# Kernel tuning notes

Hardware: AMD Instinct MI355X
Metric: run time of the kernel (lower is better)

## Reference

```python
import jax, jax.numpy as jnp
import numpy as np

K_HOPS = 3  # spektral TAGConv default
BN_EPS = 1e-3  # keras BatchNormalization default epsilon


def _propagate(x, edge_src, edge_dst, edge_weight, n_nodes):
    # y[dst] += w * x[src]  (sparse adjacency @ x)
    msg = x[edge_src] * edge_weight[:, None]
    return jax.ops.segment_sum(msg, edge_dst, num_segments=n_nodes)


def _tag_conv(x, edge_src, edge_dst, edge_weight, W, b):
    n = x.shape[0]
    hops = [x]
    h = x
    for _ in range(K_HOPS):
        h = _propagate(h, edge_src, edge_dst, edge_weight, n)
        hops.append(h)
    # concat hops along features then dense combine: [N, F*(K+1)] @ [F*(K+1), C]
    return jnp.concatenate(hops, axis=-1) @ W + b


def setup_inputs() -> dict:
    key = jax.random.key(0)
    ks = jax.random.split(key, 6)
    N, F, E, H, L = 20000, 2000, 640000, 128, 15
    x = jax.random.normal(ks[0], (N, F), dtype=jnp.float32)
    edge_src = jax.random.randint(ks[1], (E,), 0, N, dtype=jnp.int32)
    edge_dst = jax.random.randint(ks[2], (E,), 0, N, dtype=jnp.int32)
    # normalized adjacency weights, roughly 1/avg_degree scale
    edge_weight = jax.random.uniform(ks[3], (E,), dtype=jnp.float32) / 32.0
    W1 = jax.random.normal(ks[4], (F * (K_HOPS + 1), H), dtype=jnp.float32) * (1.0 / np.sqrt(F * (K_HOPS + 1)))
    b1 = jnp.zeros((H,), dtype=jnp.float32)
    gamma = jnp.ones((H,), dtype=jnp.float32)
    beta = jnp.zeros((H,), dtype=jnp.float32)
    moving_mean = jnp.zeros((H,), dtype=jnp.float32)
    moving_var = jnp.ones((H,), dtype=jnp.float32)
    W2 = jax.random.normal(ks[5], (H * (K_HOPS + 1), L), dtype=jnp.float32) * (1.0 / np.sqrt(H * (K_HOPS + 1)))
    b2 = jnp.zeros((L,), dtype=jnp.float32)
    return {"x": x, "edge_src": edge_src, "edge_dst": edge_dst, "edge_weight": edge_weight,
            "W1": W1, "b1": b1, "gamma": gamma, "beta": beta,
            "moving_mean": moving_mean, "moving_var": moving_var, "W2": W2, "b2": b2}


def reference(x, edge_src, edge_dst, edge_weight, W1, b1, gamma, beta,
              moving_mean, moving_var, W2, b2):
    # training=False: Dropout is identity, BN uses moving statistics
    h = _tag_conv(x, edge_src, edge_dst, edge_weight, W1, b1)
    h = (h - moving_mean) * jax.lax.rsqrt(moving_var + BN_EPS) * gamma + beta
    h = jax.nn.relu(h)
    z = _tag_conv(h, edge_src, edge_dst, edge_weight, W2, b2)
    return z
```

## Files before the change

kernel.cpp:

```cpp
#include <hip/hip_runtime.h>
#include <hip/hip_bf16.h>
#include <cstdint>
#include <cstddef>

#define N_NODES 20000
#define F_IN    2000
#define H_DIM   128
#define L_DIM   15
#define K_PAD   2048
#define N1      512
#define BM      128
#define BN      128
#define BK      32
#define I_TILES 157

typedef __attribute__((ext_vector_type(4))) float f32x4;
typedef __attribute__((ext_vector_type(8))) short s16x8;
typedef __attribute__((ext_vector_type(8))) unsigned short u16x8;

__device__ __forceinline__ unsigned short f2bf(float f) {
  unsigned int u = __float_as_uint(f);
  u += 0x7fff + ((u >> 16) & 1);
  return (unsigned short)(u >> 16);
}

__device__ __forceinline__ unsigned int pkbf(float a, float b) {
  union { __hip_bfloat162 h; unsigned int u; } cv;
  cv.h = __float22bfloat162_rn(make_float2(a, b));
  return cv.u;
}

__device__ __forceinline__ float2 bf2f(unsigned int u) {
  float2 r;
  r.x = __uint_as_float(u << 16);
  r.y = __uint_as_float(u & 0xffff0000u);
  return r;
}

__global__ __launch_bounds__(256) void k_cvt_x(const float* __restrict__ x,
                                               unsigned short* __restrict__ xb) {
  unsigned int t = blockIdx.x * 256u + threadIdx.x;
  unsigned int row = t >> 8;
  unsigned int colB = (t & 255u) * 8u;
  u16x8 o = {0, 0, 0, 0, 0, 0, 0, 0};
  if (colB < F_IN) {
    const float4 a = *(const float4*)(x + (size_t)row * F_IN + colB);
    const float4 b = *(const float4*)(x + (size_t)row * F_IN + colB + 4);
    o[0] = f2bf(a.x); o[1] = f2bf(a.y); o[2] = f2bf(a.z); o[3] = f2bf(a.w);
    o[4] = f2bf(b.x); o[5] = f2bf(b.y); o[6] = f2bf(b.z); o[7] = f2bf(b.w);
  }
  *(u16x8*)(xb + (size_t)t * 8) = o;
}

__global__ __launch_bounds__(256) void k_cvt_w1(const float* __restrict__ W1,
                                                unsigned short* __restrict__ bt) {
  __shared__ unsigned short tile[128 * 67];
  const int hop = blockIdx.x >> 5;
  const int k0  = (blockIdx.x & 31) * 64;
  const int t = threadIdx.x;
#pragma unroll
  for (int it = 0; it < 8; ++it) {
    int f4 = it * 256 + t;
    int r  = f4 >> 5;
    int c4 = f4 & 31;
    int k = k0 + r;
    float4 v = make_float4(0.f, 0.f, 0.f, 0.f);
    if (k < F_IN) v = *(const float4*)(W1 + (size_t)(hop * F_IN + k) * H_DIM + c4 * 4);
    tile[(c4 * 4 + 0) * 67 + r] = f2bf(v.x);
    tile[(c4 * 4 + 1) * 67 + r] = f2bf(v.y);
    tile[(c4 * 4 + 2) * 67 + r] = f2bf(v.z);
    tile[(c4 * 4 + 3) * 67 + r] = f2bf(v.w);
  }
  __syncthreads();
  const int c = t >> 1, kh = (t & 1) * 32;
  unsigned short* dst = bt + (size_t)(hop * 128 + c) * K_PAD + k0 + kh;
  const unsigned short* srcp = tile + c * 67 + kh;
#pragma unroll
  for (int q = 0; q < 4; ++q) {
    u16x8 o;
#pragma unroll
    for (int e = 0; e < 8; ++e) o[e] = srcp[q * 8 + e];
    *(u16x8*)(dst + q * 8) = o;
  }
}

__global__ __launch_bounds__(256) void k_gemm1(const unsigned short* __restrict__ A,
                                               const unsigned short* __restrict__ B,
                                               float* __restrict__ C0) {
  __shared__ unsigned short As[BM * BK];
  __shared__ unsigned short Bs[BN * BK];
  const int b = blockIdx.x;
  const int i_tile = (b & 7) + 8 * (b >> 6);
  const int mid = (b >> 3) & 7;
  const int j_tile = mid & 3;
  const int ks = mid >> 2;
  if (i_tile >= I_TILES) return;
  const int rowA0 = i_tile * BM;
  const int colB0 = j_tile * BN;
  const int tid  = threadIdx.x;
  const int lane = tid & 63;
  const int wave = tid >> 6;
  const int wm = (wave >> 1) * 64;
  const int wn = (wave & 1) * 64;
  const int quad = lane >> 4;
  const int l15  = lane & 15;
  f32x4 acc[4][4] = {};

  const int kend = ks ? F_IN : 1024;
  for (int kt = ks * 1024; kt < kend; kt += BK) {
#pragma unroll
    for (int r = 0; r < 2; ++r) {
      int c = r * 256 + tid;
      int row = c >> 2;
      int kc = (c & 3) * 8;
      const unsigned short* ga = A + (size_t)(rowA0 + row) * K_PAD + kt + kc;
      __builtin_amdgcn_global_load_lds((const __attribute__((address_space(1))) void*)ga,
                                       (__attribute__((address_space(3))) void*)(As + c * 8),
                                       16, 0, 0);
      const unsigned short* gb = B + (size_t)(colB0 + row) * K_PAD + kt + kc;
      __builtin_amdgcn_global_load_lds((const __attribute__((address_space(1))) void*)gb,
                                       (__attribute__((address_space(3))) void*)(Bs + c * 8),
                                       16, 0, 0);
    }
    __syncthreads();
    s16x8 af[4], bfr[4];
#pragma unroll
    for (int i = 0; i < 4; ++i)
      af[i] = *(const s16x8*)(As + (wm + i * 16 + l15) * BK + quad * 8);
#pragma unroll
    for (int j = 0; j < 4; ++j)
      bfr[j] = *(const s16x8*)(Bs + (wn + j * 16 + l15) * BK + quad * 8);
#pragma unroll
    for (int i = 0; i < 4; ++i)
#pragma unroll
      for (int j = 0; j < 4; ++j)
        acc[i][j] = __builtin_amdgcn_mfma_f32_16x16x32_bf16(af[i], bfr[j], acc[i][j], 0, 0, 0);
    __syncthreads();
  }

#pragma unroll
  for (int i = 0; i < 4; ++i) {
    int row0 = rowA0 + wm + i * 16 + quad * 4;
#pragma unroll
    for (int j = 0; j < 4; ++j) {
      int col = colB0 + wn + j * 16 + l15;
#pragma unroll
      for (int r = 0; r < 4; ++r) {
        int row = row0 + r;
        if (row < N_NODES)
          unsafeAtomicAdd(&C0[(size_t)row * N1 + col], acc[i][j][r]);
      }
    }
  }
}

__global__ __launch_bounds__(256) void k_mkYb3(const float* __restrict__ C0,
                                               unsigned short* __restrict__ Yb3) {
  unsigned int t = blockIdx.x * 256u + threadIdx.x;
  unsigned int row = t >> 5;
  unsigned int c4 = (t & 31u) * 4u;
  float4 s = *(const float4*)(C0 + (size_t)row * N1 + 384 + c4);
  *(uint2*)(Yb3 + (size_t)row * H_DIM + c4) = make_uint2(pkbf(s.x, s.y), pkbf(s.z, s.w));
}

__global__ __launch_bounds__(256) void k_hist(const int* __restrict__ dst,
                                              int* __restrict__ deg, int E) {
  int i = blockIdx.x * 256 + threadIdx.x;
  int e = i * 4;
  if (e + 4 <= E) {
    int4 d4 = *(const int4*)(dst + e);
    atomicAdd(&deg[d4.x], 1); atomicAdd(&deg[d4.y], 1);
    atomicAdd(&deg[d4.z], 1); atomicAdd(&deg[d4.w], 1);
  } else {
    for (; e < E; ++e) atomicAdd(&deg[dst[e]], 1);
  }
}

__global__ __launch_bounds__(1024) void k_scan(const int* __restrict__ deg,
                                               int* __restrict__ rowStart,
                                               int* __restrict__ cursor) {
  __shared__ int sums[1024];
  const int t = threadIdx.x;
  const int chunk = (N_NODES + 1023) / 1024;
  int lo = t * chunk;
  int hi = lo + chunk; if (hi > N_NODES) hi = N_NODES;
  int s = 0;
  for (int i = lo; i < hi; ++i) s += deg[i];
  sums[t] = s;
  __syncthreads();
  for (int off = 1; off < 1024; off <<= 1) {
    int v = sums[t];
    int u = (t >= off) ? sums[t - off] : 0;
    __syncthreads();
    sums[t] = v + u;
    __syncthreads();
  }
  int run = sums[t] - s;
  for (int i = lo; i < hi; ++i) {
    rowStart[i] = run; cursor[i] = run; run += deg[i];
  }
  if (t == 1023) rowStart[N_NODES] = run;
}

__global__ __launch_bounds__(256) void k_scatter(const int* __restrict__ src,
                                                 const int* __restrict__ dst,
                                                 const float* __restrict__ w,
                                                 int* cursor,
                                                 int2* __restrict__ eSW, int E) {
  int e = blockIdx.x * 256 + threadIdx.x;
  if (e >= E) return;
  int p = atomicAdd(&cursor[dst[e]], 1);
  eSW[p] = make_int2(src[e], __float_as_int(w[e]));
}

__global__ __launch_bounds__(256) void k_prop128c(const int* __restrict__ rowStart,
    const int2* __restrict__ eSW,
    const unsigned short* __restrict__ gsrc,
    const float* __restrict__ addv, int addStride, int addOff,
    unsigned short* __restrict__ outb, float* __restrict__ outf,
    const float* __restrict__ b1, const float* __restrict__ gamma,
    const float* __restrict__ beta, const float* __restrict__ mean,
    const float* __restrict__ var, int doBN) {
  __shared__ float red[2][128];
  const int lane = threadIdx.x & 63;
  const int wave = threadIdx.x >> 6;
  const int rb = wave >> 1;
  const int h  = wave & 1;
  const int d = blockIdx.x * 2 + rb;
  const int s0 = rowStart[d], s1 = rowStart[d + 1];
  const int c2 = lane * 2;
  float ax = 0.f, ay = 0.f;
  int j = s0 + h;
  for (; j + 6 < s1; j += 8) {
    int2 e0 = eSW[j], e1 = eSW[j + 2], e2 = eSW[j + 4], e3 = eSW[j + 6];
    unsigned int g0 = *(const unsigned int*)(gsrc + (size_t)e0.x * H_DIM + c2);
    unsigned int g1 = *(const unsigned int*)(gsrc + (size_t)e1.x * H_DIM + c2);
    unsigned int g2 = *(const unsigned int*)(gsrc + (size_t)e2.x * H_DIM + c2);
    unsigned int g3 = *(const unsigned int*)(gsrc + (size_t)e3.x * H_DIM + c2);
    float2 v0 = bf2f(g0), v1 = bf2f(g1), v2 = bf2f(g2), v3 = bf2f(g3);
    float w0 = __int_as_float(e0.y), w1 = __int_as_float(e1.y);
    float w2 = __int_as_float(e2.y), w3 = __int_as_float(e3.y);
    ax = fmaf(w0, v0.x, ax); ay = fmaf(w0, v0.y, ay);
    ax = fmaf(w1, v1.x, ax); ay = fmaf(w1, v1.y, ay);
    ax = fmaf(w2, v2.x, ax); ay = fmaf(w2, v2.y, ay);
    ax = fmaf(w3, v3.x, ax); ay = fmaf(w3, v3.y, ay);
  }
  for (; j < s1; j += 2) {
    int2 e = eSW[j];
    float2 v = bf2f(*(const unsigned int*)(gsrc + (size_t)e.x * H_DIM + c2));
    float w = __int_as_float(e.y);
    ax = fmaf(w, v.x, ax); ay = fmaf(w, v.y, ay);
  }
  if (h) { red[rb][c2] = ax; red[rb][c2 + 1] = ay; }
  __syncthreads();
  if (h) return;
  ax += red[rb][c2]; ay += red[rb][c2 + 1];
  float2 av = *(const float2*)(addv + (size_t)d * addStride + addOff + c2);
  float r0 = av.x + ax, r1 = av.y + ay;
  if (doBN) {
    float2 bb = *(const float2*)(b1 + c2);
    float2 gg = *(const float2*)(gamma + c2);
    float2 be = *(const float2*)(beta + c2);
    float2 mm = *(const float2*)(mean + c2);
    float2 vv = *(const float2*)(var + c2);
    r0 = (r0 + bb.x - mm.x) * rsqrtf(vv.x + 1e-3f) * gg.x + be.x;
    r1 = (r1 + bb.y - mm.y) * rsqrtf(vv.y + 1e-3f) * gg.y + be.y;
    r0 = r0 > 0.f ? r0 : 0.f;
    r1 = r1 > 0.f ? r1 : 0.f;
    *(float2*)(outf + (size_t)d * H_DIM + c2) = make_float2(r0, r1);
  } else {
    *(unsigned int*)(outb + (size_t)d * H_DIM + c2) = pkbf(r0, r1);
  }
}

__global__ __launch_bounds__(256) void k_gemm2(const float* __restrict__ Hh,
                                               const float* __restrict__ W2,
                                               float* __restrict__ Y2) {
  __shared__ float w2s[512 * 15];
  for (int i = threadIdx.x; i < 512 * 15; i += 256) w2s[i] = W2[i];
  __syncthreads();
  const int c = threadIdx.x & 63;
  const int d = blockIdx.x * 4 + (threadIdx.x >> 6);
  if (c >= 60 || d >= N_NODES) return;
  const int hop = c / 15, j = c % 15;
  const float4* hr4 = (const float4*)(Hh + (size_t)d * H_DIM);
  float acc = 0.f;
#pragma unroll 8
  for (int k4 = 0; k4 < 32; ++k4) {
    float4 h = hr4[k4];
    const float* wp = w2s + ((hop << 7) + k4 * 4) * 15 + j;
    acc = fmaf(h.x, wp[0],  acc);
    acc = fmaf(h.y, wp[15], acc);
    acc = fmaf(h.z, wp[30], acc);
    acc = fmaf(h.w, wp[45], acc);
  }
  Y2[(size_t)d * 60 + c] = acc;
}

__global__ __launch_bounds__(256) void k_prop15(const int* __restrict__ rowStart,
    const int2* __restrict__ eSW,
    const float* __restrict__ in, int inStride, int inOff,
    const float* __restrict__ addv, int addStride, int addOff,
    const float* __restrict__ bias, float* __restrict__ out) {
  const int f = threadIdx.x & 15;
  const int d = blockIdx.x * 16 + (threadIdx.x >> 4);
  if (f >= 15) return;
  const int s0 = rowStart[d], s1 = rowStart[d + 1];
  float acc = 0.f;
  int j = s0;
  for (; j + 4 <= s1; j += 4) {
    int2 e0 = eSW[j], e1 = eSW[j + 1], e2 = eSW[j + 2], e3 = eSW[j + 3];
    float v0 = in[(size_t)e0.x * inStride + inOff + f];
    float v1 = in[(size_t)e1.x * inStride + inOff + f];
    float v2 = in[(size_t)e2.x * inStride + inOff + f];
    float v3 = in[(size_t)e3.x * inStride + inOff + f];
    acc = fmaf(__int_as_float(e0.y), v0, acc);
    acc = fmaf(__int_as_float(e1.y), v1, acc);
    acc = fmaf(__int_as_float(e2.y), v2, acc);
    acc = fmaf(__int_as_float(e3.y), v3, acc);
  }
  for (; j < s1; ++j) {
    int2 e = eSW[j];
    acc = fmaf(__int_as_float(e.y), in[(size_t)e.x * inStride + inOff + f], acc);
  }
  float b = bias ? bias[f] : 0.f;
  out[(size_t)d * 15 + f] = addv[(size_t)d * addStride + addOff + f] + acc + b;
}

extern "C" void kernel_launch(void* const* d_in, const int* in_sizes, int n_in,
                              void* d_out, int out_size, void* d_ws, size_t ws_size,
                              hipStream_t stream) {
  const float* x     = (const float*)d_in[0];
  const int*   esrc  = (const int*)d_in[1];
  const int*   edst  = (const int*)d_in[2];
  const float* ew    = (const float*)d_in[3];
  const float* W1    = (const float*)d_in[4];
  const float* b1    = (const float*)d_in[5];
  const float* gamma = (const float*)d_in[6];
  const float* beta  = (const float*)d_in[7];
  const float* mmean = (const float*)d_in[8];
  const float* mvar  = (const float*)d_in[9];
  const float* W2    = (const float*)d_in[10];
  const float* b2    = (const float*)d_in[11];
  const int E = in_sizes[1];
  char* ws = (char*)d_ws;

  unsigned short* xb  = (unsigned short*)(ws);
  float*          C0  = (float*)(ws + 81920000);
  unsigned short* w1r = (unsigned short*)(ws + 122880000);
  int2*           eSW = (int2*)(ws + 124977152);
  int*       deg      = (int*)(ws + 130097152);
  int*       rowStart = (int*)(ws + 130177280);
  int*       cursor   = (int*)(ws + 130257408);
  unsigned short* Yb3 = (unsigned short*)(ws);
  unsigned short* P   = (unsigned short*)(ws + 5120000);
  unsigned short* Q   = (unsigned short*)(ws + 10240000);
  float*          Hb  = (float*)(ws + 15360000);
  float*          Y2  = (float*)(ws + 25600000);
  float*          zP  = (float*)(ws + 30400000);
  float*          zQ  = (float*)(ws + 31600000);
  float*          Y   = C0;
  float*          zout = (float*)d_out;

  hipMemsetAsync(deg, 0, N_NODES * sizeof(int), stream);
  hipMemsetAsync(C0, 0, (size_t)N_NODES * N1 * sizeof(float), stream);

  k_hist<<<(E / 4 + 255) / 256 + 1, 256, 0, stream>>>(edst, deg, E);
  k_scan<<<1, 1024, 0, stream>>>(deg, rowStart, cursor);
  k_scatter<<<(E + 255) / 256, 256, 0, stream>>>(esrc, edst, ew, cursor, eSW, E);

  k_cvt_x<<<(N_NODES * K_PAD / 8) / 256, 256, 0, stream>>>(x, xb);
  k_cvt_w1<<<128, 256, 0, stream>>>(W1, w1r);
  k_gemm1<<<1280, 256, 0, stream>>>(xb, w1r, C0);
  k_mkYb3<<<(N_NODES * 32) / 256, 256, 0, stream>>>(C0, Yb3);

  k_prop128c<<<N_NODES / 2, 256, 0, stream>>>(rowStart, eSW, Yb3, Y, N1, 2 * H_DIM,
                                              P, nullptr, b1, gamma, beta, mmean, mvar, 0);
  k_prop128c<<<N_NODES / 2, 256, 0, stream>>>(rowStart, eSW, P, Y, N1, 1 * H_DIM,
                                              Q, nullptr, b1, gamma, beta, mmean, mvar, 0);
  k_prop128c<<<N_NODES / 2, 256, 0, stream>>>(rowStart, eSW, Q, Y, N1, 0,
                                              nullptr, Hb, b1, gamma, beta, mmean, mvar, 1);

  k_gemm2<<<N_NODES / 4, 256, 0, stream>>>(Hb, W2, Y2);
  k_prop15<<<N_NODES / 16, 256, 0, stream>>>(rowStart, eSW, Y2, 60, 45, Y2, 60, 30, nullptr, zP);
  k_prop15<<<N_NODES / 16, 256, 0, stream>>>(rowStart, eSW, zP, 15, 0, Y2, 60, 15, nullptr, zQ);
  k_prop15<<<N_NODES / 16, 256, 0, stream>>>(rowStart, eSW, zQ, 15, 0, Y2, 60, 0, b2, zout);
}
```

Before: 643.3 us.

## Drop split-K atomics in gemm1, fuse bf16 output, restructure propagation kernel

The first GEMM no longer splits K across two blocks with atomic adds into a zeroed buffer. Each block now covers the full K range and writes plain stores, with the fourth column tile written directly as bf16, so the memset and the separate conversion kernel go away. The 128-wide propagation kernel now gives one wave per node, with lanes split into two halves reducing by shuffle instead of shared memory, and it software-pipelines the edge and gather loads with 4-wide loads per lane. The cost is half as many GEMM blocks, which means less parallelism and longer per-block K loops, plus higher register pressure in the pipelined gather.

```diff
diff --git a/kernel.cpp b/kernel.cpp
--- a/kernel.cpp
+++ b/kernel.cpp
@@ -8,7 +8,7 @@
 #define H_DIM   128
 #define L_DIM   15
 #define K_PAD   2048
-#define N1      512
+#define YS      384
 #define BM      128
 #define BN      128
 #define BK      32
@@ -86,14 +86,13 @@
 
 __global__ __launch_bounds__(256) void k_gemm1(const unsigned short* __restrict__ A,
                                                const unsigned short* __restrict__ B,
-                                               float* __restrict__ C0) {
+                                               float* __restrict__ Y,
+                                               unsigned short* __restrict__ Yb3) {
   __shared__ unsigned short As[BM * BK];
   __shared__ unsigned short Bs[BN * BK];
   const int b = blockIdx.x;
-  const int i_tile = (b & 7) + 8 * (b >> 6);
-  const int mid = (b >> 3) & 7;
-  const int j_tile = mid & 3;
-  const int ks = mid >> 2;
+  const int i_tile = (b & 7) + 8 * (b >> 5);
+  const int j_tile = (b >> 3) & 3;
   if (i_tile >= I_TILES) return;
   const int rowA0 = i_tile * BM;
   const int colB0 = j_tile * BN;
@@ -106,8 +105,7 @@
   const int l15  = lane & 15;
   f32x4 acc[4][4] = {};
 
-  const int kend = ks ? F_IN : 1024;
-  for (int kt = ks * 1024; kt < kend; kt += BK) {
+  for (int kt = 0; kt < K_PAD; kt += BK) {
 #pragma unroll
     for (int r = 0; r < 2; ++r) {
       int c = r * 256 + tid;
@@ -143,24 +141,19 @@
     int row0 = rowA0 + wm + i * 16 + quad * 4;
 #pragma unroll
     for (int j = 0; j < 4; ++j) {
-      int col = colB0 + wn + j * 16 + l15;
+      int col16 = wn + j * 16 + l15;
 #pragma unroll
       for (int r = 0; r < 4; ++r) {
         int row = row0 + r;
-        if (row < N_NODES)
-          unsafeAtomicAdd(&C0[(size_t)row * N1 + col], acc[i][j][r]);
+        if (row < N_NODES) {
+          if (j_tile < 3)
+            Y[(size_t)row * YS + colB0 + col16] = acc[i][j][r];
+          else
+            Yb3[(size_t)row * H_DIM + col16] = f2bf(acc[i][j][r]);
+        }
       }
     }
   }
-}
-
-__global__ __launch_bounds__(256) void k_mkYb3(const float* __restrict__ C0,
-                                               unsigned short* __restrict__ Yb3) {
-  unsigned int t = blockIdx.x * 256u + threadIdx.x;
-  unsigned int row = t >> 5;
-  unsigned int c4 = (t & 31u) * 4u;
-  float4 s = *(const float4*)(C0 + (size_t)row * N1 + 384 + c4);
-  *(uint2*)(Yb3 + (size_t)row * H_DIM + c4) = make_uint2(pkbf(s.x, s.y), pkbf(s.z, s.w));
 }
 
 __global__ __launch_bounds__(256) void k_hist(const int* __restrict__ dst,
@@ -213,7 +206,7 @@
   eSW[p] = make_int2(src[e], __float_as_int(w[e]));
 }
 
-__global__ __launch_bounds__(256) void k_prop128c(const int* __restrict__ rowStart,
+__global__ __launch_bounds__(256) void k_prop128d(const int* __restrict__ rowStart,
     const int2* __restrict__ eSW,
     const unsigned short* __restrict__ gsrc,
     const float* __restrict__ addv, int addStride, int addOff,
@@ -221,55 +214,87 @@
     const float* __restrict__ b1, const float* __restrict__ gamma,
     const float* __restrict__ beta, const float* __restrict__ mean,
     const float* __restrict__ var, int doBN) {
-  __shared__ float red[2][128];
   const int lane = threadIdx.x & 63;
   const int wave = threadIdx.x >> 6;
-  const int rb = wave >> 1;
-  const int h  = wave & 1;
-  const int d = blockIdx.x * 2 + rb;
+  const int h   = lane >> 5;
+  const int sub = lane & 31;
+  const int d = blockIdx.x * 4 + wave;
   const int s0 = rowStart[d], s1 = rowStart[d + 1];
-  const int c2 = lane * 2;
-  float ax = 0.f, ay = 0.f;
-  int j = s0 + h;
-  for (; j + 6 < s1; j += 8) {
-    int2 e0 = eSW[j], e1 = eSW[j + 2], e2 = eSW[j + 4], e3 = eSW[j + 6];
-    unsigned int g0 = *(const unsigned int*)(gsrc + (size_t)e0.x * H_DIM + c2);
-    unsigned int g1 = *(const unsigned int*)(gsrc + (size_t)e1.x * H_DIM + c2);
-    unsigned int g2 = *(const unsigned int*)(gsrc + (size_t)e2.x * H_DIM + c2);
-    unsigned int g3 = *(const unsigned int*)(gsrc + (size_t)e3.x * H_DIM + c2);
-    float2 v0 = bf2f(g0), v1 = bf2f(g1), v2 = bf2f(g2), v3 = bf2f(g3);
-    float w0 = __int_as_float(e0.y), w1 = __int_as_float(e1.y);
-    float w2 = __int_as_float(e2.y), w3 = __int_as_float(e3.y);
-    ax = fmaf(w0, v0.x, ax); ay = fmaf(w0, v0.y, ay);
-    ax = fmaf(w1, v1.x, ax); ay = fmaf(w1, v1.y, ay);
-    ax = fmaf(w2, v2.x, ax); ay = fmaf(w2, v2.y, ay);
-    ax = fmaf(w3, v3.x, ax); ay = fmaf(w3, v3.y, ay);
-  }
-  for (; j < s1; j += 2) {
-    int2 e = eSW[j];
-    float2 v = bf2f(*(const unsigned int*)(gsrc + (size_t)e.x * H_DIM + c2));
+  f32x4 acc = {0.f, 0.f, 0.f, 0.f};
+
+  const int nb = (s1 - s0) >> 3;
+  int j = s0;
+  int2 ed0[4], ed1[4];
+  uint2 g0[4];
+  if (nb > 0) {
+#pragma unroll
+    for (int i = 0; i < 4; ++i) ed0[i] = eSW[j + 2 * i + h];
+#pragma unroll
+    for (int i = 0; i < 4; ++i)
+      g0[i] = *(const uint2*)(gsrc + (size_t)ed0[i].x * H_DIM + sub * 4);
+#pragma unroll
+    for (int i = 0; i < 4; ++i)
+      ed1[i] = (nb > 1) ? eSW[j + 8 + 2 * i + h] : ed0[i];
+  }
+  for (int bb = 0; bb < nb; ++bb) {
+    uint2 g1[4];
+    if (bb + 1 < nb) {
+#pragma unroll
+      for (int i = 0; i < 4; ++i)
+        g1[i] = *(const uint2*)(gsrc + (size_t)ed1[i].x * H_DIM + sub * 4);
+    }
+    int2 ed2[4];
+    if (bb + 2 < nb) {
+#pragma unroll
+      for (int i = 0; i < 4; ++i) ed2[i] = eSW[j + 16 + 2 * i + h];
+    }
+#pragma unroll
+    for (int i = 0; i < 4; ++i) {
+      float w = __int_as_float(ed0[i].y);
+      float2 lo = bf2f(g0[i].x), hi = bf2f(g0[i].y);
+      acc.x = fmaf(w, lo.x, acc.x); acc.y = fmaf(w, lo.y, acc.y);
+      acc.z = fmaf(w, hi.x, acc.z); acc.w = fmaf(w, hi.y, acc.w);
+    }
+#pragma unroll
+    for (int i = 0; i < 4; ++i) { ed0[i] = ed1[i]; g0[i] = g1[i]; }
+    if (bb + 2 < nb) {
+#pragma unroll
+      for (int i = 0; i < 4; ++i) ed1[i] = ed2[i];
+    }
+    j += 8;
+  }
+  for (int t = s0 + nb * 8 + h; t < s1; t += 2) {
+    int2 e = eSW[t];
+    uint2 g = *(const uint2*)(gsrc + (size_t)e.x * H_DIM + sub * 4);
     float w = __int_as_float(e.y);
-    ax = fmaf(w, v.x, ax); ay = fmaf(w, v.y, ay);
-  }
-  if (h) { red[rb][c2] = ax; red[rb][c2 + 1] = ay; }
-  __syncthreads();
+    float2 lo = bf2f(g.x), hi = bf2f(g.y);
+    acc.x = fmaf(w, lo.x, acc.x); acc.y = fmaf(w, lo.y, acc.y);
+    acc.z = fmaf(w, hi.x, acc.z); acc.w = fmaf(w, hi.y, acc.w);
+  }
+  acc.x += __shfl_xor(acc.x, 32);
+  acc.y += __shfl_xor(acc.y, 32);
+  acc.z += __shfl_xor(acc.z, 32);
+  acc.w += __shfl_xor(acc.w, 32);
   if (h) return;
-  ax += red[rb][c2]; ay += red[rb][c2 + 1];
-  float2 av = *(const float2*)(addv + (size_t)d * addStride + addOff + c2);
-  float r0 = av.x + ax, r1 = av.y + ay;
+  const int c4 = sub * 4;
+  float4 av = *(const float4*)(addv + (size_t)d * addStride + addOff + c4);
+  float r0 = av.x + acc.x, r1 = av.y + acc.y;
+  float r2 = av.z + acc.z, r3 = av.w + acc.w;
   if (doBN) {
-    float2 bb = *(const float2*)(b1 + c2);
-    float2 gg = *(const float2*)(gamma + c2);
-    float2 be = *(const float2*)(beta + c2);
-    float2 mm = *(const float2*)(mean + c2);
-    float2 vv = *(const float2*)(var + c2);
+    float4 bb = *(const float4*)(b1 + c4);
+    float4 gg = *(const float4*)(gamma + c4);
+    float4 be = *(const float4*)(beta + c4);
+    float4 mm = *(const float4*)(mean + c4);
+    float4 vv = *(const float4*)(var + c4);
     r0 = (r0 + bb.x - mm.x) * rsqrtf(vv.x + 1e-3f) * gg.x + be.x;
     r1 = (r1 + bb.y - mm.y) * rsqrtf(vv.y + 1e-3f) * gg.y + be.y;
-    r0 = r0 > 0.f ? r0 : 0.f;
-    r1 = r1 > 0.f ? r1 : 0.f;
-    *(float2*)(outf + (size_t)d * H_DIM + c2) = make_float2(r0, r1);
+    r2 = (r2 + bb.z - mm.z) * rsqrtf(vv.z + 1e-3f) * gg.z + be.z;
+    r3 = (r3 + bb.w - mm.w) * rsqrtf(vv.w + 1e-3f) * gg.w + be.w;
+    r0 = r0 > 0.f ? r0 : 0.f; r1 = r1 > 0.f ? r1 : 0.f;
+    r2 = r2 > 0.f ? r2 : 0.f; r3 = r3 > 0.f ? r3 : 0.f;
+    *(float4*)(outf + (size_t)d * H_DIM + c4) = make_float4(r0, r1, r2, r3);
   } else {
-    *(unsigned int*)(outb + (size_t)d * H_DIM + c2) = pkbf(r0, r1);
+    *(uint2*)(outb + (size_t)d * H_DIM + c4) = make_uint2(pkbf(r0, r1), pkbf(r2, r3));
   }
 }
 
@@ -346,24 +371,22 @@
   char* ws = (char*)d_ws;
 
   unsigned short* xb  = (unsigned short*)(ws);
-  float*          C0  = (float*)(ws + 81920000);
-  unsigned short* w1r = (unsigned short*)(ws + 122880000);
-  int2*           eSW = (int2*)(ws + 124977152);
-  int*       deg      = (int*)(ws + 130097152);
-  int*       rowStart = (int*)(ws + 130177280);
-  int*       cursor   = (int*)(ws + 130257408);
-  unsigned short* Yb3 = (unsigned short*)(ws);
-  unsigned short* P   = (unsigned short*)(ws + 5120000);
-  unsigned short* Q   = (unsigned short*)(ws + 10240000);
-  float*          Hb  = (float*)(ws + 15360000);
-  float*          Y2  = (float*)(ws + 25600000);
-  float*          zP  = (float*)(ws + 30400000);
-  float*          zQ  = (float*)(ws + 31600000);
-  float*          Y   = C0;
+  float*          Y   = (float*)(ws + 81920000);
+  unsigned short* Yb3 = (unsigned short*)(ws + 112640000);
+  unsigned short* w1r = (unsigned short*)(ws + 117760000);
+  int2*           eSW = (int2*)(ws + 119857152);
+  int*       deg      = (int*)(ws + 124977152);
+  int*       rowStart = (int*)(ws + 125057280);
+  int*       cursor   = (int*)(ws + 125137408);
+  unsigned short* P   = (unsigned short*)(ws);
+  unsigned short* Q   = (unsigned short*)(ws + 5120000);
+  float*          Hb  = (float*)(ws + 10240000);
+  float*          Y2  = (float*)(ws + 20480000);
+  float*          zP  = (float*)(ws + 25280000);
+  float*          zQ  = (float*)(ws + 26480000);
   float*          zout = (float*)d_out;
 
   hipMemsetAsync(deg, 0, N_NODES * sizeof(int), stream);
-  hipMemsetAsync(C0, 0, (size_t)N_NODES * N1 * sizeof(float), stream);
 
   k_hist<<<(E / 4 + 255) / 256 + 1, 256, 0, stream>>>(edst, deg, E);
   k_scan<<<1, 1024, 0, stream>>>(deg, rowStart, cursor);
@@ -371,14 +394,13 @@
 
   k_cvt_x<<<(N_NODES * K_PAD / 8) / 256, 256, 0, stream>>>(x, xb);
   k_cvt_w1<<<128, 256, 0, stream>>>(W1, w1r);
-  k_gemm1<<<1280, 256, 0, stream>>>(xb, w1r, C0);
-  k_mkYb3<<<(N_NODES * 32) / 256, 256, 0, stream>>>(C0, Yb3);
-
-  k_prop128c<<<N_NODES / 2, 256, 0, stream>>>(rowStart, eSW, Yb3, Y, N1, 2 * H_DIM,
+  k_gemm1<<<640, 256, 0, stream>>>(xb, w1r, Y, Yb3);
+
+  k_prop128d<<<N_NODES / 4, 256, 0, stream>>>(rowStart, eSW, Yb3, Y, YS, 256,
                                               P, nullptr, b1, gamma, beta, mmean, mvar, 0);
-  k_prop128c<<<N_NODES / 2, 256, 0, stream>>>(rowStart, eSW, P, Y, N1, 1 * H_DIM,
+  k_prop128d<<<N_NODES / 4, 256, 0, stream>>>(rowStart, eSW, P, Y, YS, 128,
                                               Q, nullptr, b1, gamma, beta, mmean, mvar, 0);
-  k_prop128c<<<N_NODES / 2, 256, 0, stream>>>(rowStart, eSW, Q, Y, N1, 0,
+  k_prop128d<<<N_NODES / 4, 256, 0, stream>>>(rowStart, eSW, Q, Y, YS, 0,
                                               nullptr, Hb, b1, gamma, beta, mmean, mvar, 1);
 
   k_gemm2<<<N_NODES / 4, 256, 0, stream>>>(Hb, W2, Y2);
```

Result: faster. 606.3 us (-5.8%).
